# Optimization experiments

Measured on AMD Instinct MI355X. Metric: run time of the kernel, lower is better.

The kernel has to match this reference:

```python
import jax, jax.numpy as jnp
import numpy as np


def setup_inputs() -> dict:
    key = jax.random.key(0)
    x = jax.random.normal(key, (4096, 4096), dtype=jnp.float32)
    return {"x": x}


def reference(x):
    """IDCT (DCT-III) along the last axis, scaled by 2 as in DREAMPlace:
        out[k] = x[0] + 2 * sum_{n=1}^{N-1} x[n] * cos(pi*n*(2k+1)/(2N))
    computed via a 2N-point FFT with twiddle-factor (expk) pre-multiply.
    """
    N = x.shape[-1]
    # twiddle expk[n] = exp(j*pi*n/(2N))
    theta = (jnp.pi / (2.0 * N)) * jnp.arange(N, dtype=jnp.float32)
    expk = jax.lax.complex(jnp.cos(theta), jnp.sin(theta))  # complex64 [N]
    c = x.astype(jnp.complex64) * expk                       # [M, N]
    # zero-pad to 2N; S[k] = sum_n c[n] exp(+j*2*pi*n*k/(2N)) = conj(fft(conj(c2)))[k]
    c2 = jnp.concatenate([c, jnp.zeros_like(c)], axis=-1)    # [M, 2N]
    S = jnp.fft.fft(jnp.conj(c2))                            # Re(S) == Re(2N*ifft(c2))
    # out[k] = 2*Re(S[k]) - x[0]
    y = 2.0 * jnp.real(S[..., :N]) - x[..., :1]
    return y.astype(x.dtype)
```

## Files before the change

kernel.cpp:

```cpp
#include <hip/hip_runtime.h>
#include <stdint.h>


#define Md 4096
#define Nfull 4096
#define Ph 2048
#define Kh 2048
#define BM 128
#define BN 128
#define BK 32
#define NKB 64
#define TILE 4096

typedef short bf16x8 __attribute__((ext_vector_type(8)));
typedef float floatx4 __attribute__((ext_vector_type(4)));
typedef unsigned short ushort_t;

__device__ __forceinline__ ushort_t f2bf(float f) {
  union { float f; uint32_t u; } v; v.f = f;
  uint32_t u = v.u;
  return (ushort_t)((u + 0x7fffu + ((u >> 16) & 1u)) >> 16);
}

__global__ __launch_bounds__(256) void prep_kernel(const float* __restrict__ x,
                                                   ushort_t* __restrict__ Ae,
                                                   ushort_t* __restrict__ Ao,
                                                   ushort_t* __restrict__ Ce,
                                                   ushort_t* __restrict__ Co) {
  int b = blockIdx.x;
  int t = threadIdx.x;
  if (b < 2048) {
    int bm = b >> 6, kb = b & 63;
    int r = t >> 1, h = t & 1;
    const float4* xp = (const float4*)(x + (((size_t)(bm * 128 + r)) << 12) + kb * 64 + h * 32);
    float4 v0 = xp[0], v1 = xp[1], v2 = xp[2], v3 = xp[3];
    float4 v4 = xp[4], v5 = xp[5], v6 = xp[6], v7 = xp[7];
    union { ushort_t us[8]; int4 v; } e0, e1, o0, o1;
    e0.us[0] = f2bf(v0.x); o0.us[0] = f2bf(v0.y);
    e0.us[1] = f2bf(v0.z); o0.us[1] = f2bf(v0.w);
    e0.us[2] = f2bf(v1.x); o0.us[2] = f2bf(v1.y);
    e0.us[3] = f2bf(v1.z); o0.us[3] = f2bf(v1.w);
    e0.us[4] = f2bf(v2.x); o0.us[4] = f2bf(v2.y);
    e0.us[5] = f2bf(v2.z); o0.us[5] = f2bf(v2.w);
    e0.us[6] = f2bf(v3.x); o0.us[6] = f2bf(v3.y);
    e0.us[7] = f2bf(v3.z); o0.us[7] = f2bf(v3.w);
    e1.us[0] = f2bf(v4.x); o1.us[0] = f2bf(v4.y);
    e1.us[1] = f2bf(v4.z); o1.us[1] = f2bf(v4.w);
    e1.us[2] = f2bf(v5.x); o1.us[2] = f2bf(v5.y);
    e1.us[3] = f2bf(v5.z); o1.us[3] = f2bf(v5.w);
    e1.us[4] = f2bf(v6.x); o1.us[4] = f2bf(v6.y);
    e1.us[5] = f2bf(v6.z); o1.us[5] = f2bf(v6.w);
    e1.us[6] = f2bf(v7.x); o1.us[6] = f2bf(v7.y);
    e1.us[7] = f2bf(v7.z); o1.us[7] = f2bf(v7.w);
    size_t tb = ((size_t)(bm * 64 + kb)) << 12;
    int c0 = (2 * h) * 1024 + r * 8;
    int c1 = c0 + 1024;
    *(int4*)(Ae + tb + c0) = e0.v;
    *(int4*)(Ae + tb + c1) = e1.v;
    *(int4*)(Ao + tb + c0) = o0.v;
    *(int4*)(Ao + tb + c1) = o1.v;
  } else {
    int b2 = b - 2048;
    int plane = b2 >> 10;
    int bn = (b2 & 1023) >> 6, kb = b2 & 63;
    ushort_t* T = plane ? Co : Ce;
    size_t tb = ((size_t)(bn * 64 + kb)) << 12;
    const float s = 3.14159265358979f / 8192.0f;
#pragma unroll
    for (int half = 0; half < 2; ++half) {
      int cc = t + half * 256;
      int g = cc >> 7, r = cc & 127;
      int p = bn * 128 + r;
      int tp = 2 * p + 1;
      int ni = kb * 32 + g * 8;
      union { ushort_t us[8]; int4 v; } pk;
#pragma unroll
      for (int jj = 0; jj < 8; ++jj) {
        int n = 2 * (ni + jj) + plane;
        int ang = (n * tp) & 16383;
        float c = (n == 0) ? 1.0f : 2.0f * __cosf(s * (float)ang);
        pk.us[jj] = f2bf(c);
      }
      *(int4*)(T + tb + cc * 8) = pk.v;
    }
  }
}

__global__ __launch_bounds__(256, 2) void gemm_fused(const ushort_t* __restrict__ Ae,
                                                     const ushort_t* __restrict__ Ao,
                                                     const ushort_t* __restrict__ Ce,
                                                     const ushort_t* __restrict__ Co,
                                                     float* __restrict__ out) {
  __shared__ __align__(16) ushort_t S[32768];

  const int tid = threadIdx.x;
  const int wid = tid >> 6;
  const int lane = tid & 63;

  const int bm = blockIdx.y;
  const int bn = blockIdx.x;

  const int wm = (wid & 1) * 64;
  const int wn = (wid >> 1) * 64;
  const int lrow = lane & 15;

  floatx4 accE[4][4] = {};
  floatx4 accO[4][4] = {};

  const int lb = wid * 512;
  const ushort_t* pAe = Ae + (((size_t)bm * NKB) << 12) + (tid << 3);
  const ushort_t* pAo = Ao + (((size_t)bm * NKB) << 12) + (tid << 3);
  const ushort_t* pBe = Ce + (((size_t)bn * NKB) << 12) + (tid << 3);
  const ushort_t* pBo = Co + (((size_t)bn * NKB) << 12) + (tid << 3);

#define GLDS(src, dst) __builtin_amdgcn_global_load_lds( \
      (const __attribute__((address_space(1))) void*)(src), \
      (__attribute__((address_space(3))) void*)(dst), 16, 0, 0)

#define STAGE(bufoff, t) do { \
    size_t so_ = ((size_t)(t)) << 12; \
    _Pragma("unroll") \
    for (int i_ = 0; i_ < 2; ++i_) { \
      GLDS(pAe + so_ + i_ * 2048, S + (bufoff) + i_ * 2048 + lb); \
      GLDS(pAo + so_ + i_ * 2048, S + (bufoff) + 4096 + i_ * 2048 + lb); \
      GLDS(pBe + so_ + i_ * 2048, S + (bufoff) + 8192 + i_ * 2048 + lb); \
      GLDS(pBo + so_ + i_ * 2048, S + (bufoff) + 12288 + i_ * 2048 + lb); \
    } } while (0)

  const int g1024 = (lane >> 4) << 10;
  const int rb8 = lrow << 3;

#define COMPUTE(bufoff) do { \
    bf16x8 bE_[4], bO_[4]; \
    _Pragma("unroll") \
    for (int f_ = 0; f_ < 4; ++f_) { \
      int off_ = (bufoff) + g1024 + rb8 + ((wn + f_ * 16) << 3); \
      bE_[f_] = *(const bf16x8*)(S + 8192 + off_); \
      bO_[f_] = *(const bf16x8*)(S + 12288 + off_); \
    } \
    __builtin_amdgcn_s_setprio(1); \
    _Pragma("unroll") \
    for (int im_ = 0; im_ < 4; ++im_) { \
      int off_ = (bufoff) + g1024 + rb8 + ((wm + im_ * 16) << 3); \
      bf16x8 aE_ = *(const bf16x8*)(S + off_); \
      bf16x8 aO_ = *(const bf16x8*)(S + 4096 + off_); \
      _Pragma("unroll") \
      for (int jn_ = 0; jn_ < 4; ++jn_) { \
        accE[im_][jn_] = __builtin_amdgcn_mfma_f32_16x16x32_bf16(aE_, bE_[jn_], accE[im_][jn_], 0, 0, 0); \
        accO[im_][jn_] = __builtin_amdgcn_mfma_f32_16x16x32_bf16(aO_, bO_[jn_], accO[im_][jn_], 0, 0, 0); \
      } \
    } \
    __builtin_amdgcn_s_setprio(0); \
  } while (0)

#define WAITVM(n) do { \
    asm volatile("s_waitcnt vmcnt(" #n ")" ::: "memory"); \
    __builtin_amdgcn_sched_barrier(0); \
  } while (0)

  STAGE(0, 0);
  STAGE(16384, 1);

  for (int t = 0; t < NKB - 2; ++t) {
    const int cur = (t & 1) << 14;
    WAITVM(8);
    __builtin_amdgcn_s_barrier();
    COMPUTE(cur);
    __builtin_amdgcn_s_barrier();
    STAGE(cur, t + 2);
  }
  WAITVM(8);
  __builtin_amdgcn_s_barrier();
  COMPUTE(0);
  WAITVM(0);
  __builtin_amdgcn_s_barrier();
  COMPUTE(16384);

#undef GLDS
#undef STAGE
#undef COMPUTE
#undef WAITVM

#pragma unroll
  for (int im = 0; im < 4; ++im) {
    int rb = bm * BM + wm + im * 16 + (lane >> 4) * 4;
#pragma unroll
    for (int jn = 0; jn < 4; ++jn) {
      int p = bn * BN + wn + jn * 16 + lrow;
      float* lo = out + (size_t)rb * Nfull + p;
      float* hi = out + (size_t)rb * Nfull + (Nfull - 1 - p);
#pragma unroll
      for (int r = 0; r < 4; ++r) {
        float e = accE[im][jn][r];
        float o = accO[im][jn][r];
        lo[(size_t)r * Nfull] = e + o;
        hi[(size_t)r * Nfull] = e - o;
      }
    }
  }
}

extern "C" void kernel_launch(void* const* d_in, const int* in_sizes, int n_in,
                              void* d_out, int out_size, void* d_ws, size_t ws_size,
                              hipStream_t stream) {
  const float* x = (const float*)d_in[0];
  float* out = (float*)d_out;
  ushort_t* Ae = (ushort_t*)d_ws;
  ushort_t* Ao = Ae + (size_t)8 * 1024 * 1024;
  ushort_t* Ce = Ao + (size_t)8 * 1024 * 1024;
  ushort_t* Co = Ce + (size_t)4 * 1024 * 1024;

  prep_kernel<<<4096, 256, 0, stream>>>(x, Ae, Ao, Ce, Co);

  dim3 grid(Ph / BN, Md / BM);
  gemm_fused<<<grid, 256, 0, stream>>>(Ae, Ao, Ce, Co, out);
}
```

Measured before the change: 176.5 us.

## Enlarge GEMM tile to 256 rows with 8 waves and triple-buffered LDS

The fused even/odd GEMM now uses 512-thread blocks covering 256 rows by 128 columns. Each wave handles either the even or the odd plane for an 8x4 fragment grid, and LDS is split into three stage buffers loaded ahead in a triple-buffered pipeline. Partial even/odd accumulators are exchanged through LDS at the end so the symmetric lo/hi outputs can be formed. The aim is more reuse of loaded tiles and better overlap of loads with MFMA work, at the cost of lower occupancy (one block per CU) and an extra LDS exchange in the epilogue.

Measured after the change: 266.5 us. +51.0%, slower.

```diff
diff --git a/kernel.cpp b/kernel.cpp
--- a/kernel.cpp
+++ b/kernel.cpp
@@ -6,11 +6,10 @@
 #define Nfull 4096
 #define Ph 2048
 #define Kh 2048
-#define BM 128
+#define BM 256
 #define BN 128
 #define BK 32
 #define NKB 64
-#define TILE 4096
 
 typedef short bf16x8 __attribute__((ext_vector_type(8)));
 typedef float floatx4 __attribute__((ext_vector_type(4)));
@@ -86,69 +85,67 @@
   }
 }
 
-__global__ __launch_bounds__(256, 2) void gemm_fused(const ushort_t* __restrict__ Ae,
+__global__ __launch_bounds__(512, 1) void gemm_fused(const ushort_t* __restrict__ Ae,
                                                      const ushort_t* __restrict__ Ao,
                                                      const ushort_t* __restrict__ Ce,
                                                      const ushort_t* __restrict__ Co,
                                                      float* __restrict__ out) {
-  __shared__ __align__(16) ushort_t S[32768];
+  __shared__ __align__(16) ushort_t T0[24576];
+  __shared__ __align__(16) ushort_t T1[24576];
+  __shared__ __align__(16) ushort_t T2[24576];
 
   const int tid = threadIdx.x;
   const int wid = tid >> 6;
   const int lane = tid & 63;
 
+  const int br = wid & 1;
+  const int ch = (wid >> 1) & 1;
+  const int rh = wid >> 2;
+  const int lrow = lane & 15;
+  const int lq = lane >> 4;
+  const int g1024 = lq << 10;
+  const int rb8 = lrow << 3;
+  const int abase = br * 8192 + rh * 4096;
+  const int bbase = 16384 + br * 4096 + ch * 512;
+
   const int bm = blockIdx.y;
   const int bn = blockIdx.x;
 
-  const int wm = (wid & 1) * 64;
-  const int wn = (wid >> 1) * 64;
-  const int lrow = lane & 15;
-
-  floatx4 accE[4][4] = {};
-  floatx4 accO[4][4] = {};
-
-  const int lb = wid * 512;
-  const ushort_t* pAe = Ae + (((size_t)bm * NKB) << 12) + (tid << 3);
-  const ushort_t* pAo = Ao + (((size_t)bm * NKB) << 12) + (tid << 3);
-  const ushort_t* pBe = Ce + (((size_t)bn * NKB) << 12) + (tid << 3);
-  const ushort_t* pBo = Co + (((size_t)bn * NKB) << 12) + (tid << 3);
+  floatx4 acc[8][4] = {};
+
+  const ushort_t* pA0 = Ae + (((size_t)(128 * bm)) << 12) + (tid << 3);
+  const ushort_t* pA1 = pA0 + ((size_t)64 << 12);
+  const ushort_t* pO0 = Ao + (((size_t)(128 * bm)) << 12) + (tid << 3);
+  const ushort_t* pO1 = pO0 + ((size_t)64 << 12);
+  const ushort_t* pBe = Ce + (((size_t)(64 * bn)) << 12) + (tid << 3);
+  const ushort_t* pBo = Co + (((size_t)(64 * bn)) << 12) + (tid << 3);
 
 #define GLDS(src, dst) __builtin_amdgcn_global_load_lds( \
       (const __attribute__((address_space(1))) void*)(src), \
       (__attribute__((address_space(3))) void*)(dst), 16, 0, 0)
 
-#define STAGE(bufoff, t) do { \
-    size_t so_ = ((size_t)(t)) << 12; \
+#define STAGE(SB, tt) do { \
+    size_t so_ = ((size_t)(tt)) << 12; \
+    GLDS(pA0 + so_, SB + (tid << 3)); \
+    GLDS(pA1 + so_, SB + 4096 + (tid << 3)); \
+    GLDS(pO0 + so_, SB + 8192 + (tid << 3)); \
+    GLDS(pO1 + so_, SB + 12288 + (tid << 3)); \
+    GLDS(pBe + so_, SB + 16384 + (tid << 3)); \
+    GLDS(pBo + so_, SB + 20480 + (tid << 3)); \
+  } while (0)
+
+#define COMPUTE(SB) do { \
+    bf16x8 b_[4]; \
     _Pragma("unroll") \
-    for (int i_ = 0; i_ < 2; ++i_) { \
-      GLDS(pAe + so_ + i_ * 2048, S + (bufoff) + i_ * 2048 + lb); \
-      GLDS(pAo + so_ + i_ * 2048, S + (bufoff) + 4096 + i_ * 2048 + lb); \
-      GLDS(pBe + so_ + i_ * 2048, S + (bufoff) + 8192 + i_ * 2048 + lb); \
-      GLDS(pBo + so_ + i_ * 2048, S + (bufoff) + 12288 + i_ * 2048 + lb); \
-    } } while (0)
-
-  const int g1024 = (lane >> 4) << 10;
-  const int rb8 = lrow << 3;
-
-#define COMPUTE(bufoff) do { \
-    bf16x8 bE_[4], bO_[4]; \
-    _Pragma("unroll") \
-    for (int f_ = 0; f_ < 4; ++f_) { \
-      int off_ = (bufoff) + g1024 + rb8 + ((wn + f_ * 16) << 3); \
-      bE_[f_] = *(const bf16x8*)(S + 8192 + off_); \
-      bO_[f_] = *(const bf16x8*)(S + 12288 + off_); \
-    } \
+    for (int jn_ = 0; jn_ < 4; ++jn_) \
+      b_[jn_] = *(const bf16x8*)(SB + bbase + g1024 + rb8 + jn_ * 128); \
     __builtin_amdgcn_s_setprio(1); \
     _Pragma("unroll") \
-    for (int im_ = 0; im_ < 4; ++im_) { \
-      int off_ = (bufoff) + g1024 + rb8 + ((wm + im_ * 16) << 3); \
-      bf16x8 aE_ = *(const bf16x8*)(S + off_); \
-      bf16x8 aO_ = *(const bf16x8*)(S + 4096 + off_); \
+    for (int im_ = 0; im_ < 8; ++im_) { \
+      bf16x8 a_ = *(const bf16x8*)(SB + abase + g1024 + rb8 + im_ * 128); \
       _Pragma("unroll") \
-      for (int jn_ = 0; jn_ < 4; ++jn_) { \
-        accE[im_][jn_] = __builtin_amdgcn_mfma_f32_16x16x32_bf16(aE_, bE_[jn_], accE[im_][jn_], 0, 0, 0); \
-        accO[im_][jn_] = __builtin_amdgcn_mfma_f32_16x16x32_bf16(aO_, bO_[jn_], accO[im_][jn_], 0, 0, 0); \
-      } \
+      for (int jn_ = 0; jn_ < 4; ++jn_) \
+        acc[im_][jn_] = __builtin_amdgcn_mfma_f32_16x16x32_bf16(a_, b_[jn_], acc[im_][jn_], 0, 0, 0); \
     } \
     __builtin_amdgcn_s_setprio(0); \
   } while (0)
@@ -158,41 +155,75 @@
     __builtin_amdgcn_sched_barrier(0); \
   } while (0)
 
-  STAGE(0, 0);
-  STAGE(16384, 1);
-
-  for (int t = 0; t < NKB - 2; ++t) {
-    const int cur = (t & 1) << 14;
-    WAITVM(8);
+  STAGE(T0, 0);
+  STAGE(T1, 1);
+
+  for (int tt = 0; tt < 60; tt += 3) {
+    WAITVM(6);
     __builtin_amdgcn_s_barrier();
-    COMPUTE(cur);
+    COMPUTE(T0);
+    STAGE(T2, tt + 2);
+    WAITVM(6);
     __builtin_amdgcn_s_barrier();
-    STAGE(cur, t + 2);
-  }
-  WAITVM(8);
-  __builtin_amdgcn_s_barrier();
-  COMPUTE(0);
+    COMPUTE(T1);
+    STAGE(T0, tt + 3);
+    WAITVM(6);
+    __builtin_amdgcn_s_barrier();
+    COMPUTE(T2);
+    STAGE(T1, tt + 4);
+  }
+  WAITVM(6);
+  __builtin_amdgcn_s_barrier();
+  COMPUTE(T0);
+  STAGE(T2, 62);
+  WAITVM(6);
+  __builtin_amdgcn_s_barrier();
+  COMPUTE(T1);
+  STAGE(T0, 63);
+  WAITVM(6);
+  __builtin_amdgcn_s_barrier();
+  COMPUTE(T2);
   WAITVM(0);
   __builtin_amdgcn_s_barrier();
-  COMPUTE(16384);
+  COMPUTE(T0);
 
 #undef GLDS
 #undef STAGE
 #undef COMPUTE
 #undef WAITVM
 
-#pragma unroll
-  for (int im = 0; im < 4; ++im) {
-    int rb = bm * BM + wm + im * 16 + (lane >> 4) * 4;
+  __syncthreads();
+  float* my = (wid < 3) ? ((float*)T0 + wid * 4096)
+            : (wid < 6) ? ((float*)T1 + (wid - 3) * 4096)
+                        : ((float*)T2 + (wid - 6) * 4096);
+  const int pw = wid ^ 1;
+  const float* pr = (pw < 3) ? ((const float*)T0 + pw * 4096)
+                  : (pw < 6) ? ((const float*)T1 + (pw - 3) * 4096)
+                             : ((const float*)T2 + (pw - 6) * 4096);
+  {
+    const int dbase = (br ^ 1) << 2;
+#pragma unroll
+    for (int i4 = 0; i4 < 4; ++i4)
+#pragma unroll
+      for (int jn = 0; jn < 4; ++jn)
+        *(floatx4*)(my + (i4 * 4 + jn) * 256 + lane * 4) = acc[dbase + i4][jn];
+  }
+  __syncthreads();
+  const int kbase = br << 2;
+#pragma unroll
+  for (int i4 = 0; i4 < 4; ++i4) {
+    int im = kbase + i4;
+    int rb = bm * BM + rh * 128 + im * 16 + lq * 4;
 #pragma unroll
     for (int jn = 0; jn < 4; ++jn) {
-      int p = bn * BN + wn + jn * 16 + lrow;
+      floatx4 oth = *(const floatx4*)(pr + (i4 * 4 + jn) * 256 + lane * 4);
+      int p = bn * BN + ch * 64 + jn * 16 + lrow;
       float* lo = out + (size_t)rb * Nfull + p;
       float* hi = out + (size_t)rb * Nfull + (Nfull - 1 - p);
 #pragma unroll
       for (int r = 0; r < 4; ++r) {
-        float e = accE[im][jn][r];
-        float o = accO[im][jn][r];
+        float e = br ? oth[r] : acc[im][jn][r];
+        float o = br ? acc[im][jn][r] : oth[r];
         lo[(size_t)r * Nfull] = e + o;
         hi[(size_t)r * Nfull] = e - o;
       }
@@ -213,5 +244,5 @@
   prep_kernel<<<4096, 256, 0, stream>>>(x, Ae, Ao, Ce, Co);
 
   dim3 grid(Ph / BN, Md / BM);
-  gemm_fused<<<grid, 256, 0, stream>>>(Ae, Ao, Ce, Co, out);
-}
+  gemm_fused<<<grid, 512, 0, stream>>>(Ae, Ao, Ce, Co, out);
+}
```

## Switch GEMM to 32x32x16 MFMA, swizzle block order, use cosine recurrence in prep

Applied to the files above, without the earlier changes.

The main GEMM now uses 32x32x16 bf16 MFMA tiles instead of 16x16x32, with re-derived LDS fragment offsets and output row mapping. This cuts the number of MFMA issues and LDS fragment loads per K step. Block IDs are also swizzled so that consecutive blocks share A and B tiles in cache. The prep kernel builds cosine tables with a Chebyshev recurrence instead of one __cosf per element, which may slightly change bf16 rounding of the coefficients.

Result: slower. 183.3 us (+3.9%).

```diff
diff --git a/kernel.cpp b/kernel.cpp
--- a/kernel.cpp
+++ b/kernel.cpp
@@ -10,10 +10,9 @@
 #define BN 128
 #define BK 32
 #define NKB 64
-#define TILE 4096
 
 typedef short bf16x8 __attribute__((ext_vector_type(8)));
-typedef float floatx4 __attribute__((ext_vector_type(4)));
+typedef float floatx16 __attribute__((ext_vector_type(16)));
 typedef unsigned short ushort_t;
 
 __device__ __forceinline__ ushort_t f2bf(float f) {
@@ -73,14 +72,20 @@
       int p = bn * 128 + r;
       int tp = 2 * p + 1;
       int ni = kb * 32 + g * 8;
+      int n0 = 2 * ni + plane;
+      float c0 = __cosf(s * (float)((n0 * tp) & 16383));
+      float c1 = __cosf(s * (float)(((n0 + 2) * tp) & 16383));
+      float T2 = 2.0f * __cosf(s * (float)(2 * tp));
       union { ushort_t us[8]; int4 v; } pk;
-#pragma unroll
-      for (int jj = 0; jj < 8; ++jj) {
-        int n = 2 * (ni + jj) + plane;
-        int ang = (n * tp) & 16383;
-        float c = (n == 0) ? 1.0f : 2.0f * __cosf(s * (float)ang);
-        pk.us[jj] = f2bf(c);
+      pk.us[0] = f2bf(2.0f * c0);
+      pk.us[1] = f2bf(2.0f * c1);
+#pragma unroll
+      for (int jj = 2; jj < 8; ++jj) {
+        float c2 = __builtin_fmaf(T2, c1, -c0);
+        pk.us[jj] = f2bf(2.0f * c2);
+        c0 = c1; c1 = c2;
       }
+      if (plane == 0 && ni == 0) pk.us[0] = f2bf(1.0f);
       *(int4*)(T + tb + cc * 8) = pk.v;
     }
   }
@@ -97,15 +102,18 @@
   const int wid = tid >> 6;
   const int lane = tid & 63;
 
-  const int bm = blockIdx.y;
-  const int bn = blockIdx.x;
+  const int id = blockIdx.y * gridDim.x + blockIdx.x;
+  const int swz = (id & 7) * 64 + (id >> 3);
+  const int bn = swz & 15;
+  const int bm = swz >> 4;
 
   const int wm = (wid & 1) * 64;
   const int wn = (wid >> 1) * 64;
-  const int lrow = lane & 15;
-
-  floatx4 accE[4][4] = {};
-  floatx4 accO[4][4] = {};
+  const int l31 = lane & 31;
+  const int lhi = lane >> 5;
+
+  floatx16 accE[2][2] = {};
+  floatx16 accO[2][2] = {};
 
   const int lb = wid * 512;
   const ushort_t* pAe = Ae + (((size_t)bm * NKB) << 12) + (tid << 3);
@@ -127,30 +135,31 @@
       GLDS(pBo + so_ + i_ * 2048, S + (bufoff) + 12288 + i_ * 2048 + lb); \
     } } while (0)
 
-  const int g1024 = (lane >> 4) << 10;
-  const int rb8 = lrow << 3;
-
 #define COMPUTE(bufoff) do { \
-    bf16x8 bE_[4], bO_[4]; \
     _Pragma("unroll") \
-    for (int f_ = 0; f_ < 4; ++f_) { \
-      int off_ = (bufoff) + g1024 + rb8 + ((wn + f_ * 16) << 3); \
-      bE_[f_] = *(const bf16x8*)(S + 8192 + off_); \
-      bO_[f_] = *(const bf16x8*)(S + 12288 + off_); \
+    for (int kk_ = 0; kk_ < 2; ++kk_) { \
+      const int g_ = ((lhi + 2 * kk_) << 10) + (bufoff); \
+      bf16x8 bE_[2], bO_[2]; \
+      _Pragma("unroll") \
+      for (int jn_ = 0; jn_ < 2; ++jn_) { \
+        int off_ = g_ + ((wn + jn_ * 32 + l31) << 3); \
+        bE_[jn_] = *(const bf16x8*)(S + 8192 + off_); \
+        bO_[jn_] = *(const bf16x8*)(S + 12288 + off_); \
+      } \
+      __builtin_amdgcn_s_setprio(1); \
+      _Pragma("unroll") \
+      for (int im_ = 0; im_ < 2; ++im_) { \
+        int off_ = g_ + ((wm + im_ * 32 + l31) << 3); \
+        bf16x8 aE_ = *(const bf16x8*)(S + off_); \
+        bf16x8 aO_ = *(const bf16x8*)(S + 4096 + off_); \
+        _Pragma("unroll") \
+        for (int jn_ = 0; jn_ < 2; ++jn_) { \
+          accE[im_][jn_] = __builtin_amdgcn_mfma_f32_32x32x16_bf16(aE_, bE_[jn_], accE[im_][jn_], 0, 0, 0); \
+          accO[im_][jn_] = __builtin_amdgcn_mfma_f32_32x32x16_bf16(aO_, bO_[jn_], accO[im_][jn_], 0, 0, 0); \
+        } \
+      } \
+      __builtin_amdgcn_s_setprio(0); \
     } \
-    __builtin_amdgcn_s_setprio(1); \
-    _Pragma("unroll") \
-    for (int im_ = 0; im_ < 4; ++im_) { \
-      int off_ = (bufoff) + g1024 + rb8 + ((wm + im_ * 16) << 3); \
-      bf16x8 aE_ = *(const bf16x8*)(S + off_); \
-      bf16x8 aO_ = *(const bf16x8*)(S + 4096 + off_); \
-      _Pragma("unroll") \
-      for (int jn_ = 0; jn_ < 4; ++jn_) { \
-        accE[im_][jn_] = __builtin_amdgcn_mfma_f32_16x16x32_bf16(aE_, bE_[jn_], accE[im_][jn_], 0, 0, 0); \
-        accO[im_][jn_] = __builtin_amdgcn_mfma_f32_16x16x32_bf16(aO_, bO_[jn_], accO[im_][jn_], 0, 0, 0); \
-      } \
-    } \
-    __builtin_amdgcn_s_setprio(0); \
   } while (0)
 
 #define WAITVM(n) do { \
@@ -182,19 +191,20 @@
 #undef WAITVM
 
 #pragma unroll
-  for (int im = 0; im < 4; ++im) {
-    int rb = bm * BM + wm + im * 16 + (lane >> 4) * 4;
-#pragma unroll
-    for (int jn = 0; jn < 4; ++jn) {
-      int p = bn * BN + wn + jn * 16 + lrow;
-      float* lo = out + (size_t)rb * Nfull + p;
-      float* hi = out + (size_t)rb * Nfull + (Nfull - 1 - p);
-#pragma unroll
-      for (int r = 0; r < 4; ++r) {
+  for (int im = 0; im < 2; ++im) {
+    int rb0 = bm * BM + wm + im * 32 + 4 * lhi;
+#pragma unroll
+    for (int jn = 0; jn < 2; ++jn) {
+      int p = bn * BN + wn + jn * 32 + l31;
+      float* lo = out + p;
+      float* hi = out + (Nfull - 1 - p);
+#pragma unroll
+      for (int r = 0; r < 16; ++r) {
+        int row = rb0 + (r & 3) + 8 * (r >> 2);
         float e = accE[im][jn][r];
         float o = accO[im][jn][r];
-        lo[(size_t)r * Nfull] = e + o;
-        hi[(size_t)r * Nfull] = e - o;
+        lo[(size_t)row * Nfull] = e + o;
+        hi[(size_t)row * Nfull] = e - o;
       }
     }
   }
```
